# Optimization experiments

Hardware: AMD Instinct MI355X
Metric: run time of the kernel (lower is better)

Reference implementation:

```python
import jax, jax.numpy as jnp
import numpy as np

D_MODEL = 1024
N_HEADS = 16
D_K = D_MODEL // N_HEADS


def setup_inputs() -> dict:
    key = jax.random.key(0)
    ks = jax.random.split(key, 11)
    B, S = 2, 2048
    scale = 1.0 / np.sqrt(D_MODEL)
    inp = {
        "q": jax.random.normal(ks[0], (B, S, D_MODEL), jnp.float32),
        "k": jax.random.normal(ks[1], (B, S, D_MODEL), jnp.float32),
        "v": jax.random.normal(ks[2], (B, S, D_MODEL), jnp.float32),
        "W_q": jax.random.normal(ks[3], (D_MODEL, D_MODEL), jnp.float32) * scale,
        "b_q": jnp.zeros((D_MODEL,), jnp.float32),
        "W_k": jax.random.normal(ks[4], (D_MODEL, D_MODEL), jnp.float32) * scale,
        "b_k": jnp.zeros((D_MODEL,), jnp.float32),
        "W_v": jax.random.normal(ks[5], (D_MODEL, D_MODEL), jnp.float32) * scale,
        "b_v": jnp.zeros((D_MODEL,), jnp.float32),
        "W_o": jax.random.normal(ks[6], (D_MODEL, D_MODEL), jnp.float32) * scale,
        "b_o": jnp.zeros((D_MODEL,), jnp.float32),
    }
    return inp


def _split_heads(x):
    B, S, _ = x.shape
    return x.reshape(B, S, N_HEADS, D_K).transpose(0, 2, 1, 3)  # [B,H,S,dk]


def reference(q, k, v, W_q, b_q, W_k, b_k, W_v, b_v, W_o, b_o):
    Q = _split_heads(q @ W_q + b_q)
    K = _split_heads(k @ W_k + b_k)
    V = _split_heads(v @ W_v + b_v)
    scores = jnp.einsum("bhqd,bhkd->bhqk", Q, K) / jnp.sqrt(jnp.float32(D_K))
    attn = jax.nn.softmax(scores, axis=-1)  # [B,H,S,S]
    out = jnp.einsum("bhqk,bhkd->bhqd", attn, V)
    B, H, S, dk = out.shape
    out = out.transpose(0, 2, 1, 3).reshape(B, S, H * dk)
    return out @ W_o + b_o, attn
```

## Files before the change

kernel.cpp:

```cpp
#include <hip/hip_runtime.h>
#include <hip/hip_bf16.h>

typedef __bf16 bf16x8 __attribute__((ext_vector_type(8)));
typedef float f32x4 __attribute__((ext_vector_type(4)));

#define DEV static __device__ __forceinline__

DEV unsigned short f2bf(float x) {
  union { __hip_bfloat16 b; unsigned short u; } c;
  c.b = __float2bfloat16(x);
  return c.u;
}

DEV void gload_lds16(const void* g, void* l) {
  __builtin_amdgcn_global_load_lds((const __attribute__((address_space(1))) void*)g,
                                   (__attribute__((address_space(3))) void*)l, 16, 0, 0);
}

__global__ __launch_bounds__(256) void cvt_qkv(const float* __restrict__ q,
                                               const float* __restrict__ k,
                                               const float* __restrict__ v,
                                               unsigned short* __restrict__ qb,
                                               unsigned short* __restrict__ kb,
                                               unsigned short* __restrict__ vb) {
  const float* src = blockIdx.y == 0 ? q : (blockIdx.y == 1 ? k : v);
  unsigned short* dst = blockIdx.y == 0 ? qb : (blockIdx.y == 1 ? kb : vb);
  int idx = (blockIdx.x * 256 + threadIdx.x) * 4;
  float4 xv = *(const float4*)(src + idx);
  ushort4 o;
  o.x = f2bf(xv.x); o.y = f2bf(xv.y); o.z = f2bf(xv.z); o.w = f2bf(xv.w);
  *(ushort4*)(dst + idx) = o;
}

__global__ __launch_bounds__(256) void transpose_all(const float* __restrict__ W0,
                                                     const float* __restrict__ W1,
                                                     const float* __restrict__ W2,
                                                     const float* __restrict__ W3,
                                                     unsigned short* __restrict__ T0,
                                                     unsigned short* __restrict__ T1,
                                                     unsigned short* __restrict__ T2,
                                                     unsigned short* __restrict__ T3) {
  __shared__ float t[64][68];
  int sel = blockIdx.x >> 8;
  const float* W = sel == 0 ? W0 : sel == 1 ? W1 : sel == 2 ? W2 : W3;
  unsigned short* Wt = sel == 0 ? T0 : sel == 1 ? T1 : sel == 2 ? T2 : T3;
  int tile = blockIdx.x & 255;
  int tr = tile >> 4, tc = tile & 15;
  int lr = threadIdx.x >> 4, lc4 = threadIdx.x & 15;
#pragma unroll
  for (int i = 0; i < 4; ++i) {
    int r = i * 16 + lr;
    float4 v = *(const float4*)(W + (size_t)(tr * 64 + r) * 1024 + tc * 64 + lc4 * 4);
    t[r][lc4 * 4 + 0] = v.x; t[r][lc4 * 4 + 1] = v.y;
    t[r][lc4 * 4 + 2] = v.z; t[r][lc4 * 4 + 3] = v.w;
  }
  __syncthreads();
#pragma unroll
  for (int i = 0; i < 4; ++i) {
    int r = i * 16 + lr;
    ushort4 o;
    o.x = f2bf(t[lc4 * 4 + 0][r]);
    o.y = f2bf(t[lc4 * 4 + 1][r]);
    o.z = f2bf(t[lc4 * 4 + 2][r]);
    o.w = f2bf(t[lc4 * 4 + 3][r]);
    *(ushort4*)(Wt + (size_t)(tc * 64 + r) * 1024 + tr * 64 + lc4 * 4) = o;
  }
}

DEV void gemm_core(const unsigned short* __restrict__ A, const unsigned short* __restrict__ Bt,
                   const float* __restrict__ bias, void* __restrict__ Cout,
                   float scale, int mode, int blk,
                   unsigned short* As, unsigned short* Bs) {
  const int tid = threadIdx.x;
  const int l = tid & 63, w = tid >> 6;
  const int wm = w >> 1, wn = w & 1;
  const int r15 = l & 15, kg = l >> 4;
  const int mt = blk >> 3, nt = blk & 7;

  const f32x4 fz = {0.f, 0.f, 0.f, 0.f};
  f32x4 acc[4][4];
#pragma unroll
  for (int i = 0; i < 4; ++i)
#pragma unroll
    for (int j = 0; j < 4; ++j) acc[i][j] = fz;

  for (int kt = 0; kt < 16; ++kt) {
#pragma unroll
    for (int c = 0; c < 4; ++c) {
      int chunk = c * 256 + tid;
      int row = chunk >> 3, slot = chunk & 7;
      int gsl = slot ^ (row & 7);
      gload_lds16(A + (size_t)(mt * 128 + row) * 1024 + kt * 64 + gsl * 8, As + chunk * 8);
      gload_lds16(Bt + (size_t)(nt * 128 + row) * 1024 + kt * 64 + gsl * 8, Bs + chunk * 8);
    }
    __syncthreads();
#pragma unroll
    for (int ks = 0; ks < 2; ++ks) {
      bf16x8 a[4], b[4];
      int slot = ks * 4 + kg;
#pragma unroll
      for (int i = 0; i < 4; ++i) {
        int ra = wm * 64 + i * 16 + r15;
        a[i] = *(const bf16x8*)(As + ra * 64 + (slot ^ (ra & 7)) * 8);
        int rb = wn * 64 + i * 16 + r15;
        b[i] = *(const bf16x8*)(Bs + rb * 64 + (slot ^ (rb & 7)) * 8);
      }
#pragma unroll
      for (int i = 0; i < 4; ++i)
#pragma unroll
        for (int j = 0; j < 4; ++j)
          acc[i][j] = __builtin_amdgcn_mfma_f32_16x16x32_bf16(a[i], b[j], acc[i][j], 0, 0, 0);
    }
    __syncthreads();
  }

#pragma unroll
  for (int j = 0; j < 4; ++j) {
    int gc = nt * 128 + wn * 64 + j * 16 + r15;
    float bj = bias[gc];
#pragma unroll
    for (int i = 0; i < 4; ++i) {
#pragma unroll
      for (int r = 0; r < 4; ++r) {
        int gr = mt * 128 + wm * 64 + i * 16 + kg * 4 + r;
        float val = (acc[i][j][r] + bj) * scale;
        if (mode == 2) {
          ((float*)Cout)[(size_t)gr * 1024 + gc] = val;
        } else {
          int bb = gr >> 11, s = gr & 2047, hh = gc >> 6, dk = gc & 63;
          if (mode == 0)
            ((unsigned short*)Cout)[((size_t)(bb * 16 + hh) * 2048 + s) * 64 + dk] = f2bf(val);
          else
            ((unsigned short*)Cout)[((size_t)(bb * 16 + hh) * 64 + dk) * 2048 + s] = f2bf(val);
        }
      }
    }
  }
}

__global__ __launch_bounds__(256) void gemm_qkv(const unsigned short* __restrict__ qb,
                                                const unsigned short* __restrict__ kb,
                                                const unsigned short* __restrict__ vb,
                                                const unsigned short* __restrict__ Wtq,
                                                const unsigned short* __restrict__ Wtk,
                                                const unsigned short* __restrict__ Wtv,
                                                const float* __restrict__ bq,
                                                const float* __restrict__ bk,
                                                const float* __restrict__ bv,
                                                unsigned short* __restrict__ Qh,
                                                unsigned short* __restrict__ Kh,
                                                unsigned short* __restrict__ Vt) {
  __shared__ unsigned short As[128 * 64];
  __shared__ unsigned short Bs[128 * 64];
  int sel = blockIdx.x >> 8, blk = blockIdx.x & 255;
  const unsigned short* A = sel == 0 ? qb : sel == 1 ? kb : vb;
  const unsigned short* Bt = sel == 0 ? Wtq : sel == 1 ? Wtk : Wtv;
  const float* bias = sel == 0 ? bq : sel == 1 ? bk : bv;
  void* C = sel == 0 ? (void*)Qh : sel == 1 ? (void*)Kh : (void*)Vt;
  gemm_core(A, Bt, bias, C, sel == 0 ? 0.125f : 1.0f, sel == 2 ? 1 : 0, blk, As, Bs);
}

__global__ __launch_bounds__(256) void gemm_out(const unsigned short* __restrict__ AO,
                                                const unsigned short* __restrict__ Wto,
                                                const float* __restrict__ bo,
                                                float* __restrict__ out0) {
  __shared__ unsigned short As[128 * 64];
  __shared__ unsigned short Bs[128 * 64];
  gemm_core(AO, Wto, bo, out0, 1.0f, 2, blockIdx.x, As, Bs);
}

__global__ __launch_bounds__(256, 4) void attn_kernel(const unsigned short* __restrict__ Qh,
                                                      const unsigned short* __restrict__ Kh,
                                                      const unsigned short* __restrict__ Vt,
                                                      float* __restrict__ attnO,
                                                      unsigned short* __restrict__ AO) {
  __shared__ unsigned short Pbuf[2][32 * 64];
  __shared__ float Ms[4][32], Ss[4][32];
  __shared__ float mrow[32], rrow[32];

  const int tid = threadIdx.x;
  const int l = tid & 63, w = tid >> 6;
  const int r15 = l & 15, kg = l >> 4;

  const int lb = ((int)blockIdx.x & 7) * 256 + ((int)blockIdx.x >> 3);
  const int bh = lb >> 6;
  const int q0 = (lb & 63) * 32;
  const int b = bh >> 4, h = bh & 15;

  const unsigned short* Kbase = Kh + (size_t)bh * 2048 * 64;
  const unsigned short* Vbase = Vt + (size_t)bh * 64 * 2048;

  bf16x8 aq[2][2];
#pragma unroll
  for (int j = 0; j < 2; ++j)
#pragma unroll
    for (int h2 = 0; h2 < 2; ++h2)
      aq[j][h2] = *(const bf16x8*)(Qh + ((size_t)bh * 2048 + q0 + j * 16 + r15) * 64 +
                                   (h2 * 4 + kg) * 8);

  const int krow = w * 16 + r15;
  const f32x4 z4 = {0.f, 0.f, 0.f, 0.f};

  float m2[2] = {-3e38f, -3e38f}, s2[2] = {0.f, 0.f};

  for (int kt = 0; kt < 32; ++kt) {
    const unsigned short* kp = Kbase + (size_t)(kt * 64 + krow) * 64;
    bf16x8 kf0 = *(const bf16x8*)(kp + kg * 8);
    bf16x8 kf1 = *(const bf16x8*)(kp + 32 + kg * 8);
#pragma unroll
    for (int j = 0; j < 2; ++j) {
      f32x4 sc = __builtin_amdgcn_mfma_f32_16x16x32_bf16(kf0, aq[j][0], z4, 0, 0, 0);
      sc = __builtin_amdgcn_mfma_f32_16x16x32_bf16(kf1, aq[j][1], sc, 0, 0, 0);
      float tm = fmaxf(fmaxf(sc[0], sc[1]), fmaxf(sc[2], sc[3]));
      float mn = fmaxf(m2[j], tm);
      s2[j] = s2[j] * __expf(m2[j] - mn) + __expf(sc[0] - mn) + __expf(sc[1] - mn) +
              __expf(sc[2] - mn) + __expf(sc[3] - mn);
      m2[j] = mn;
    }
  }

#pragma unroll
  for (int j = 0; j < 2; ++j) {
#pragma unroll
    for (int off = 16; off <= 32; off <<= 1) {
      float mo = __shfl_xor(m2[j], off, 64);
      float so = __shfl_xor(s2[j], off, 64);
      float mn = fmaxf(m2[j], mo);
      s2[j] = s2[j] * __expf(m2[j] - mn) + so * __expf(mo - mn);
      m2[j] = mn;
    }
    if (kg == 0) { Ms[w][j * 16 + r15] = m2[j]; Ss[w][j * 16 + r15] = s2[j]; }
  }
  __syncthreads();
  if (tid < 32) {
    float m = Ms[0][tid], s = Ss[0][tid];
#pragma unroll
    for (int ww = 1; ww < 4; ++ww) {
      float mo = Ms[ww][tid], so = Ss[ww][tid];
      float mn = fmaxf(m, mo);
      s = s * __expf(m - mn) + so * __expf(mo - mn);
      m = mn;
    }
    mrow[tid] = m;
    rrow[tid] = 1.0f / s;
  }
  __syncthreads();

  const float mq[2] = {mrow[r15], mrow[16 + r15]};
  const float rvq[2] = {rrow[r15], rrow[16 + r15]};
  const int prow = tid >> 3;
  const int pc8 = (tid & 7) * 8;
  const float rv_w = rrow[prow];
  float* attnBase = attnO + ((size_t)bh * 2048 + q0) * 2048;

  f32x4 oacc[2] = {z4, z4};
  const unsigned short* vp = Vbase + (size_t)(w * 16 + r15) * 2048;

  for (int kt = 0; kt < 32; ++kt) {
    const unsigned short* kp = Kbase + (size_t)(kt * 64 + krow) * 64;
    bf16x8 kf0 = *(const bf16x8*)(kp + kg * 8);
    bf16x8 kf1 = *(const bf16x8*)(kp + 32 + kg * 8);
    unsigned short* Pb = &Pbuf[kt & 1][0];
#pragma unroll
    for (int j = 0; j < 2; ++j) {
      f32x4 sc = __builtin_amdgcn_mfma_f32_16x16x32_bf16(kf0, aq[j][0], z4, 0, 0, 0);
      sc = __builtin_amdgcn_mfma_f32_16x16x32_bf16(kf1, aq[j][1], sc, 0, 0, 0);
      ushort4 e;
      e.x = f2bf(__expf(sc[0] - mq[j]));
      e.y = f2bf(__expf(sc[1] - mq[j]));
      e.z = f2bf(__expf(sc[2] - mq[j]));
      e.w = f2bf(__expf(sc[3] - mq[j]));
      int q = j * 16 + r15;
      int c4 = (w * 4 + kg) ^ ((q & 7) << 1);
      *(ushort4*)(Pb + q * 64 + c4 * 4) = e;
    }
    __syncthreads();
    bf16x8 av0 = *(const bf16x8*)(vp + kt * 64 + kg * 8);
    bf16x8 av1 = *(const bf16x8*)(vp + kt * 64 + 32 + kg * 8);
#pragma unroll
    for (int j = 0; j < 2; ++j) {
      int q = j * 16 + r15;
      bf16x8 pf0 = *(const bf16x8*)(Pb + q * 64 + ((kg ^ (q & 7)) * 8));
      bf16x8 pf1 = *(const bf16x8*)(Pb + q * 64 + (((4 + kg) ^ (q & 7)) * 8));
      oacc[j] = __builtin_amdgcn_mfma_f32_16x16x32_bf16(av0, pf0, oacc[j], 0, 0, 0);
      oacc[j] = __builtin_amdgcn_mfma_f32_16x16x32_bf16(av1, pf1, oacc[j], 0, 0, 0);
    }
    {
      bf16x8 pv = *(const bf16x8*)(Pb + prow * 64 + (((pc8 >> 3) ^ (prow & 7)) * 8));
      float4 o0, o1;
      o0.x = (float)pv[0] * rv_w; o0.y = (float)pv[1] * rv_w;
      o0.z = (float)pv[2] * rv_w; o0.w = (float)pv[3] * rv_w;
      o1.x = (float)pv[4] * rv_w; o1.y = (float)pv[5] * rv_w;
      o1.z = (float)pv[6] * rv_w; o1.w = (float)pv[7] * rv_w;
      float* dst = attnBase + (size_t)prow * 2048 + kt * 64 + pc8;
      *(float4*)dst = o0;
      *(float4*)(dst + 4) = o1;
    }
  }

#pragma unroll
  for (int j = 0; j < 2; ++j) {
    float rv = rvq[j];
    ushort4 o;
    o.x = f2bf(oacc[j][0] * rv);
    o.y = f2bf(oacc[j][1] * rv);
    o.z = f2bf(oacc[j][2] * rv);
    o.w = f2bf(oacc[j][3] * rv);
    int q = q0 + j * 16 + r15;
    *(ushort4*)(AO + ((size_t)(b * 2048 + q)) * 1024 + h * 64 + w * 16 + kg * 4) = o;
  }
}

extern "C" void kernel_launch(void* const* d_in, const int* in_sizes, int n_in,
                              void* d_out, int out_size, void* d_ws, size_t ws_size,
                              hipStream_t stream) {
  const float* q  = (const float*)d_in[0];
  const float* k  = (const float*)d_in[1];
  const float* v  = (const float*)d_in[2];
  const float* Wq = (const float*)d_in[3];
  const float* bq = (const float*)d_in[4];
  const float* Wk = (const float*)d_in[5];
  const float* bk = (const float*)d_in[6];
  const float* Wv = (const float*)d_in[7];
  const float* bvp = (const float*)d_in[8];
  const float* Wo = (const float*)d_in[9];
  const float* bo = (const float*)d_in[10];

  char* wsb = (char*)d_ws;
  const size_t MB = (size_t)1 << 20;
  unsigned short* qb  = (unsigned short*)(wsb + 0 * MB);
  unsigned short* kbp = (unsigned short*)(wsb + 8 * MB);
  unsigned short* vbp = (unsigned short*)(wsb + 16 * MB);
  unsigned short* Wtq = (unsigned short*)(wsb + 24 * MB);
  unsigned short* Wtk = (unsigned short*)(wsb + 26 * MB);
  unsigned short* Wtv = (unsigned short*)(wsb + 28 * MB);
  unsigned short* Wto = (unsigned short*)(wsb + 30 * MB);
  unsigned short* Qh  = (unsigned short*)(wsb + 32 * MB);
  unsigned short* Kh  = (unsigned short*)(wsb + 40 * MB);
  unsigned short* Vt  = (unsigned short*)(wsb + 48 * MB);
  unsigned short* AO  = (unsigned short*)(wsb + 56 * MB);

  float* out0 = (float*)d_out;
  float* attnO = out0 + (size_t)2 * 2048 * 1024;

  cvt_qkv<<<dim3(4096, 3), 256, 0, stream>>>(q, k, v, qb, kbp, vbp);
  transpose_all<<<1024, 256, 0, stream>>>(Wq, Wk, Wv, Wo, Wtq, Wtk, Wtv, Wto);
  gemm_qkv<<<768, 256, 0, stream>>>(qb, kbp, vbp, Wtq, Wtk, Wtv, bq, bk, bvp, Qh, Kh, Vt);
  attn_kernel<<<2048, 256, 0, stream>>>(Qh, Kh, Vt, attnO, AO);
  gemm_out<<<256, 256, 0, stream>>>(AO, Wto, bo, (float*)d_out);
}
```

Before: 386.7 us.

## Keep softmax probabilities in registers for PV MFMA, drop per-tile LDS barrier

The attention kernel no longer stages the bf16 probability tile through LDS with a __syncthreads every key tile. Each wave now feeds its score fragment straight into 16x16x16 MFMAs against V fragments loaded from global memory. It keeps per-wave partial outputs over all 64 head dims and reduces them across the four waves once at the end through LDS. The attention matrix is written directly from the MFMA accumulator layout, and exp is switched to exp2f with log2(e) folded into the Q projection scale. In exchange it uses more accumulator registers and smaller V loads, and the attn stores are less contiguous (16-byte chunks).

Result: slower. 472.8 us (+22.3%).

```diff
diff --git a/kernel.cpp b/kernel.cpp
--- a/kernel.cpp
+++ b/kernel.cpp
@@ -3,6 +3,8 @@
 
 typedef __bf16 bf16x8 __attribute__((ext_vector_type(8)));
 typedef float f32x4 __attribute__((ext_vector_type(4)));
+typedef short short4v __attribute__((ext_vector_type(4)));
+typedef unsigned short ushort8v __attribute__((ext_vector_type(8)));
 
 #define DEV static __device__ __forceinline__
 
@@ -157,7 +159,8 @@
   const unsigned short* Bt = sel == 0 ? Wtq : sel == 1 ? Wtk : Wtv;
   const float* bias = sel == 0 ? bq : sel == 1 ? bk : bv;
   void* C = sel == 0 ? (void*)Qh : sel == 1 ? (void*)Kh : (void*)Vt;
-  gemm_core(A, Bt, bias, C, sel == 0 ? 0.125f : 1.0f, sel == 2 ? 1 : 0, blk, As, Bs);
+  gemm_core(A, Bt, bias, C, sel == 0 ? 0.125f * 1.44269504088896f : 1.0f,
+            sel == 2 ? 1 : 0, blk, As, Bs);
 }
 
 __global__ __launch_bounds__(256) void gemm_out(const unsigned short* __restrict__ AO,
@@ -174,7 +177,7 @@
                                                       const unsigned short* __restrict__ Vt,
                                                       float* __restrict__ attnO,
                                                       unsigned short* __restrict__ AO) {
-  __shared__ unsigned short Pbuf[2][32 * 64];
+  __shared__ float Ored[4][32][68];
   __shared__ float Ms[4][32], Ss[4][32];
   __shared__ float mrow[32], rrow[32];
 
@@ -213,8 +216,8 @@
       sc = __builtin_amdgcn_mfma_f32_16x16x32_bf16(kf1, aq[j][1], sc, 0, 0, 0);
       float tm = fmaxf(fmaxf(sc[0], sc[1]), fmaxf(sc[2], sc[3]));
       float mn = fmaxf(m2[j], tm);
-      s2[j] = s2[j] * __expf(m2[j] - mn) + __expf(sc[0] - mn) + __expf(sc[1] - mn) +
-              __expf(sc[2] - mn) + __expf(sc[3] - mn);
+      s2[j] = s2[j] * exp2f(m2[j] - mn) + exp2f(sc[0] - mn) + exp2f(sc[1] - mn) +
+              exp2f(sc[2] - mn) + exp2f(sc[3] - mn);
       m2[j] = mn;
     }
   }
@@ -226,7 +229,7 @@
       float mo = __shfl_xor(m2[j], off, 64);
       float so = __shfl_xor(s2[j], off, 64);
       float mn = fmaxf(m2[j], mo);
-      s2[j] = s2[j] * __expf(m2[j] - mn) + so * __expf(mo - mn);
+      s2[j] = s2[j] * exp2f(m2[j] - mn) + so * exp2f(mo - mn);
       m2[j] = mn;
     }
     if (kg == 0) { Ms[w][j * 16 + r15] = m2[j]; Ss[w][j * 16 + r15] = s2[j]; }
@@ -238,7 +241,7 @@
     for (int ww = 1; ww < 4; ++ww) {
       float mo = Ms[ww][tid], so = Ss[ww][tid];
       float mn = fmaxf(m, mo);
-      s = s * __expf(m - mn) + so * __expf(mo - mn);
+      s = s * exp2f(m - mn) + so * exp2f(mo - mn);
       m = mn;
     }
     mrow[tid] = m;
@@ -248,66 +251,57 @@
 
   const float mq[2] = {mrow[r15], mrow[16 + r15]};
   const float rvq[2] = {rrow[r15], rrow[16 + r15]};
-  const int prow = tid >> 3;
-  const int pc8 = (tid & 7) * 8;
-  const float rv_w = rrow[prow];
   float* attnBase = attnO + ((size_t)bh * 2048 + q0) * 2048;
 
-  f32x4 oacc[2] = {z4, z4};
-  const unsigned short* vp = Vbase + (size_t)(w * 16 + r15) * 2048;
+  f32x4 oacc[2][4];
+#pragma unroll
+  for (int j = 0; j < 2; ++j)
+#pragma unroll
+    for (int d = 0; d < 4; ++d) oacc[j][d] = z4;
 
   for (int kt = 0; kt < 32; ++kt) {
     const unsigned short* kp = Kbase + (size_t)(kt * 64 + krow) * 64;
     bf16x8 kf0 = *(const bf16x8*)(kp + kg * 8);
     bf16x8 kf1 = *(const bf16x8*)(kp + 32 + kg * 8);
-    unsigned short* Pb = &Pbuf[kt & 1][0];
+    short4v vf[4];
+#pragma unroll
+    for (int d = 0; d < 4; ++d)
+      vf[d] = *(const short4v*)(Vbase + (size_t)(d * 16 + r15) * 2048 + kt * 64 + w * 16 + kg * 4);
 #pragma unroll
     for (int j = 0; j < 2; ++j) {
       f32x4 sc = __builtin_amdgcn_mfma_f32_16x16x32_bf16(kf0, aq[j][0], z4, 0, 0, 0);
       sc = __builtin_amdgcn_mfma_f32_16x16x32_bf16(kf1, aq[j][1], sc, 0, 0, 0);
-      ushort4 e;
-      e.x = f2bf(__expf(sc[0] - mq[j]));
-      e.y = f2bf(__expf(sc[1] - mq[j]));
-      e.z = f2bf(__expf(sc[2] - mq[j]));
-      e.w = f2bf(__expf(sc[3] - mq[j]));
-      int q = j * 16 + r15;
-      int c4 = (w * 4 + kg) ^ ((q & 7) << 1);
-      *(ushort4*)(Pb + q * 64 + c4 * 4) = e;
-    }
-    __syncthreads();
-    bf16x8 av0 = *(const bf16x8*)(vp + kt * 64 + kg * 8);
-    bf16x8 av1 = *(const bf16x8*)(vp + kt * 64 + 32 + kg * 8);
-#pragma unroll
-    for (int j = 0; j < 2; ++j) {
-      int q = j * 16 + r15;
-      bf16x8 pf0 = *(const bf16x8*)(Pb + q * 64 + ((kg ^ (q & 7)) * 8));
-      bf16x8 pf1 = *(const bf16x8*)(Pb + q * 64 + (((4 + kg) ^ (q & 7)) * 8));
-      oacc[j] = __builtin_amdgcn_mfma_f32_16x16x32_bf16(av0, pf0, oacc[j], 0, 0, 0);
-      oacc[j] = __builtin_amdgcn_mfma_f32_16x16x32_bf16(av1, pf1, oacc[j], 0, 0, 0);
-    }
-    {
-      bf16x8 pv = *(const bf16x8*)(Pb + prow * 64 + (((pc8 >> 3) ^ (prow & 7)) * 8));
-      float4 o0, o1;
-      o0.x = (float)pv[0] * rv_w; o0.y = (float)pv[1] * rv_w;
-      o0.z = (float)pv[2] * rv_w; o0.w = (float)pv[3] * rv_w;
-      o1.x = (float)pv[4] * rv_w; o1.y = (float)pv[5] * rv_w;
-      o1.z = (float)pv[6] * rv_w; o1.w = (float)pv[7] * rv_w;
-      float* dst = attnBase + (size_t)prow * 2048 + kt * 64 + pc8;
-      *(float4*)dst = o0;
-      *(float4*)(dst + 4) = o1;
-    }
-  }
-
-#pragma unroll
-  for (int j = 0; j < 2; ++j) {
-    float rv = rvq[j];
-    ushort4 o;
-    o.x = f2bf(oacc[j][0] * rv);
-    o.y = f2bf(oacc[j][1] * rv);
-    o.z = f2bf(oacc[j][2] * rv);
-    o.w = f2bf(oacc[j][3] * rv);
-    int q = q0 + j * 16 + r15;
-    *(ushort4*)(AO + ((size_t)(b * 2048 + q)) * 1024 + h * 64 + w * 16 + kg * 4) = o;
+      float e0 = exp2f(sc[0] - mq[j]);
+      float e1 = exp2f(sc[1] - mq[j]);
+      float e2 = exp2f(sc[2] - mq[j]);
+      float e3 = exp2f(sc[3] - mq[j]);
+      f32x4 st = {e0 * rvq[j], e1 * rvq[j], e2 * rvq[j], e3 * rvq[j]};
+      *(f32x4*)(attnBase + (size_t)(j * 16 + r15) * 2048 + kt * 64 + w * 16 + kg * 4) = st;
+      short4v pf;
+      pf[0] = (short)f2bf(e0); pf[1] = (short)f2bf(e1);
+      pf[2] = (short)f2bf(e2); pf[3] = (short)f2bf(e3);
+#pragma unroll
+      for (int d = 0; d < 4; ++d)
+        oacc[j][d] = __builtin_amdgcn_mfma_f32_16x16x16bf16_1k(vf[d], pf, oacc[j][d], 0, 0, 0);
+    }
+  }
+
+#pragma unroll
+  for (int j = 0; j < 2; ++j)
+#pragma unroll
+    for (int d = 0; d < 4; ++d)
+      *(f32x4*)&Ored[w][j * 16 + r15][d * 16 + kg * 4] = oacc[j][d];
+  __syncthreads();
+  {
+    int q = tid >> 3, dc = (tid & 7) * 8;
+    float rv = rrow[q];
+    ushort8v o;
+#pragma unroll
+    for (int i = 0; i < 8; ++i) {
+      float s = Ored[0][q][dc + i] + Ored[1][q][dc + i] + Ored[2][q][dc + i] + Ored[3][q][dc + i];
+      o[i] = f2bf(s * rv);
+    }
+    *(ushort8v*)(AO + ((size_t)(b * 2048 + q0 + q)) * 1024 + h * 64 + dc) = o;
   }
 }
 
@@ -340,8 +334,7 @@
   unsigned short* Vt  = (unsigned short*)(wsb + 48 * MB);
   unsigned short* AO  = (unsigned short*)(wsb + 56 * MB);
 
-  float* out0 = (float*)d_out;
-  float* attnO = out0 + (size_t)2 * 2048 * 1024;
+  float* attnO = (float*)d_out + (size_t)2 * 2048 * 1024;
 
   cvt_qkv<<<dim3(4096, 3), 256, 0, stream>>>(q, k, v, qb, kbp, vbp);
   transpose_all<<<1024, 256, 0, stream>>>(Wq, Wk, Wv, Wo, Wtq, Wtk, Wtv, Wto);
```
